# Kernel tuning notes

Measured on AMD Instinct MI355X. Metric: run time of the kernel, lower is better.

The kernel has to match this reference:

```python
import jax, jax.numpy as jnp
import numpy as np

A = 128   # image height (x_shape[0])
B = 128   # image width  (x_shape[1]); must equal A for the matmuls to type-check
N = 64    # glimpse size
H_DIM = 512
BATCH = 2048


def _filterbanks(params):
    """Vectorized Gaussian filterbank construction (replaces the per-column loop).
    params: (5,) = [gt_X, gt_Y, log_var, log_dt, log_gamma].
    gt_X, gt_Y, d are detached in the original via fix_param() -> stop_gradient here.
    """
    gt_X = jax.lax.stop_gradient(params[0])
    gt_Y = jax.lax.stop_gradient(params[1])
    var = jnp.exp(params[2] + 1e-8)
    d = jax.lax.stop_gradient(jnp.exp(params[3]) * (max(A, B) - 1) / (N - 1))
    g_X = (A + 1) * (gt_X + 1) / 2
    g_Y = (B + 1) * (gt_Y + 1) / 2
    # torch.linspace(g + (-N/2-0.5)*d, g + (N-1-N/2-0.5)*d, N) == g + (i - N/2 - 0.5)*d
    offs = (jnp.arange(N, dtype=jnp.float32) - N / 2 - 0.5) * d
    mu_X = g_X + offs  # (N,)
    mu_Y = g_Y + offs  # (N,)
    a = jnp.arange(A, dtype=jnp.float32)
    b = jnp.arange(B, dtype=jnp.float32)
    F_X = jnp.exp(-(a[None, :] - mu_X[:, None]) ** 2 / (2 * var))  # (N, A)
    F_Y = jnp.exp(-(b[None, :] - mu_Y[:, None]) ** 2 / (2 * var))  # (N, B)
    # NOTE: original normalizes by the GLOBAL sum, not per-row.
    F_X = F_X / jnp.sum(F_X)
    F_Y = F_Y / jnp.sum(F_Y)
    return F_X, F_Y


def setup_inputs() -> dict:
    key = jax.random.key(0)
    k1, k2, k3, k4 = jax.random.split(key, 4)
    x = jax.random.normal(k1, (BATCH, A * B), dtype=jnp.float32)
    x_hat = jax.random.normal(k2, (BATCH, A * B), dtype=jnp.float32)
    h = jax.random.normal(k3, (BATCH, H_DIM), dtype=jnp.float32)
    # W_read: Linear(h_dim, 5). Small init so exp(log_var), exp(log_dt), exp(log_gamma) stay sane.
    W_read_w = jax.random.normal(k4, (5, H_DIM), dtype=jnp.float32) * 0.01
    W_read_b = jnp.zeros((5,), dtype=jnp.float32)
    return {"x": x, "x_hat": x_hat, "h": h, "W_read_w": W_read_w, "W_read_b": W_read_b}


def reference(x, x_hat, h, W_read_w, W_read_b):
    # params = W_read(h)[0]  -> uses only the first batch element's params (as in original)
    params = h[0] @ W_read_w.T + W_read_b  # (5,)
    gamma = jnp.exp(params[4])
    F_X, F_Y = _filterbanks(params)  # (N, A), (N, B)

    xr = x.reshape(-1, A, B)
    xh = x_hat.reshape(-1, A, B)
    # gamma * F_Y @ x @ F_X.T : (batch, N, N)
    x_filt = gamma * jnp.einsum('na,bac,mc->bnm', F_Y, xr, F_X)
    x_hat_filt = gamma * jnp.einsum('na,bac,mc->bnm', F_Y, xh, F_X)
    return jnp.concatenate([x_filt.reshape(-1, N * N), x_hat_filt.reshape(-1, N * N)], axis=1)
```

## Files before the change

kernel.cpp:

```cpp
#include <hip/hip_runtime.h>
#include <math.h>

#define A_DIM 128
#define N_G   64
#define HD    512
#define LDX   136

typedef short short8 __attribute__((ext_vector_type(8)));
typedef float floatx4 __attribute__((ext_vector_type(4)));

static __device__ __forceinline__ unsigned short f2bf(float f) {
  union { float f; unsigned u; } v; v.f = f;
  unsigned r = (v.u + 0x7fffu + ((v.u >> 16) & 1u)) >> 16;
  return (unsigned short)r;
}

__global__ __launch_bounds__(512) void fb_setup_kernel(
    const float* __restrict__ h, const float* __restrict__ Ww,
    const float* __restrict__ Wb, unsigned short* __restrict__ FXfrag,
    unsigned short* __restrict__ FYfrag) {
  __shared__ float p[5];
  __shared__ float redX[8], redY[8];
  __shared__ float invs[2];
  const int tid = threadIdx.x, wave = tid >> 6, lane = tid & 63;

  if (wave < 5) {
    float s = 0.f;
    for (int k = lane; k < HD; k += 64) s += h[k] * Ww[wave * HD + k];
#pragma unroll
    for (int off = 32; off > 0; off >>= 1) s += __shfl_down(s, off);
    if (lane == 0) p[wave] = s + Wb[wave];
  }
  __syncthreads();

  const float gX = 64.5f * (p[0] + 1.0f);
  const float gY = 64.5f * (p[1] + 1.0f);
  const float var = expf(p[2] + 1e-8f);
  const float dd = expf(p[3]) * (127.0f / 63.0f);
  const float gamma = expf(p[4]);
  const float two_var = 2.0f * var;

  float sX = 0.f, sY = 0.f;
  for (int i = tid; i < N_G * A_DIM; i += 512) {
    const int n = i >> 7, a = i & 127;
    const float off_n = ((float)n - 32.5f) * dd;
    const float tx = (float)a - (gX + off_n);
    const float ty = (float)a - (gY + off_n);
    sX += expf(-(tx * tx) / two_var);
    sY += expf(-(ty * ty) / two_var);
  }
#pragma unroll
  for (int off = 32; off > 0; off >>= 1) {
    sX += __shfl_down(sX, off);
    sY += __shfl_down(sY, off);
  }
  if (lane == 0) { redX[wave] = sX; redY[wave] = sY; }
  __syncthreads();
  if (tid == 0) {
    float tX = 0.f, tY = 0.f;
#pragma unroll
    for (int w = 0; w < 8; ++w) { tX += redX[w]; tY += redY[w]; }
    invs[0] = 1.0f / tX;
    invs[1] = gamma / tY;
  }
  __syncthreads();
  const float isX = invs[0], isYg = invs[1];

  for (int i = tid; i < 4 * 4 * 64 * 8; i += 512) {
    const int j = i & 7;
    const int ln = (i >> 3) & 63;
    const int kk = (i >> 9) & 3;
    const int tl = (i >> 11) & 3;
    const int mn = tl * 16 + (ln & 15);
    const int ca = kk * 32 + ((ln >> 4) << 3) + j;
    const float off_mn = ((float)mn - 32.5f) * dd;
    const float tx = (float)ca - (gX + off_mn);
    const float ty = (float)ca - (gY + off_mn);
    FXfrag[i] = f2bf(expf(-(tx * tx) / two_var) * isX);
    FYfrag[i] = f2bf(expf(-(ty * ty) / two_var) * isYg);
  }
}

__global__ __launch_bounds__(256) void glimpse_kernel(
    const float* __restrict__ x, const float* __restrict__ xh,
    const unsigned short* __restrict__ FXfrag,
    const unsigned short* __restrict__ FYfrag,
    float* __restrict__ out) {
  const int img = blockIdx.x;
  const int b = img >> 1, t = img & 1;
  const float* __restrict__ src = (t ? xh : x) + (size_t)b * (A_DIM * A_DIM);
  float* __restrict__ dst = out + (size_t)b * (2 * N_G * N_G) + t * (N_G * N_G);

  __shared__ __align__(16) unsigned short xs[A_DIM * LDX];
  __shared__ __align__(16) unsigned short us[N_G * LDX];

  const int tid = threadIdx.x;
  const int w = tid >> 6, lane = tid & 63;
  const int quad = lane >> 4, lm = lane & 15;

  {
    const float4* __restrict__ src4 = (const float4*)src;
#pragma unroll
    for (int it = 0; it < 16; ++it) {
      const int flat = it * 256 + tid;
      const int a = flat >> 5;
      const int c4 = (flat & 31) * 4;
      const float4 v = src4[flat];
      uint2 pk;
      pk.x = (unsigned)f2bf(v.x) | ((unsigned)f2bf(v.y) << 16);
      pk.y = (unsigned)f2bf(v.z) | ((unsigned)f2bf(v.w) << 16);
      *(uint2*)&xs[a * LDX + c4] = pk;
    }
  }
  __syncthreads();

  {
    floatx4 acc[2][4];
#pragma unroll
    for (int i = 0; i < 2; ++i)
#pragma unroll
      for (int j = 0; j < 4; ++j) acc[i][j] = (floatx4)0.f;

#pragma unroll
    for (int kk = 0; kk < 4; ++kk) {
      short8 aF[2], bF[4];
#pragma unroll
      for (int i = 0; i < 2; ++i)
        aF[i] = *(const short8*)&xs[((2 * w + i) * 16 + lm) * LDX + kk * 32 + quad * 8];
#pragma unroll
      for (int j = 0; j < 4; ++j)
        bF[j] = *(const short8*)(FXfrag + ((size_t)(j * 4 + kk) * 64 + lane) * 8);
#pragma unroll
      for (int i = 0; i < 2; ++i)
#pragma unroll
        for (int j = 0; j < 4; ++j)
          acc[i][j] = __builtin_amdgcn_mfma_f32_16x16x32_bf16(aF[i], bF[j], acc[i][j], 0, 0, 0);
    }

#pragma unroll
    for (int i = 0; i < 2; ++i)
#pragma unroll
      for (int j = 0; j < 4; ++j) {
        uint2 pk;
        pk.x = (unsigned)f2bf(acc[i][j][0]) | ((unsigned)f2bf(acc[i][j][1]) << 16);
        pk.y = (unsigned)f2bf(acc[i][j][2]) | ((unsigned)f2bf(acc[i][j][3]) << 16);
        *(uint2*)&us[(j * 16 + lm) * LDX + (2 * w + i) * 16 + quad * 4] = pk;
      }
  }
  __syncthreads();

  {
    floatx4 acc2[4];
#pragma unroll
    for (int j = 0; j < 4; ++j) acc2[j] = (floatx4)0.f;

#pragma unroll
    for (int kk = 0; kk < 4; ++kk) {
      const short8 aF = *(const short8*)(FYfrag + ((size_t)(w * 4 + kk) * 64 + lane) * 8);
#pragma unroll
      for (int mt = 0; mt < 4; ++mt) {
        const short8 bF = *(const short8*)&us[(mt * 16 + lm) * LDX + kk * 32 + quad * 8];
        acc2[mt] = __builtin_amdgcn_mfma_f32_16x16x32_bf16(aF, bF, acc2[mt], 0, 0, 0);
      }
    }

#pragma unroll
    for (int mt = 0; mt < 4; ++mt)
#pragma unroll
      for (int r = 0; r < 4; ++r)
        dst[(w * 16 + quad * 4 + r) * N_G + mt * 16 + lm] = acc2[mt][r];
  }
}

extern "C" void kernel_launch(void* const* d_in, const int* in_sizes, int n_in,
                              void* d_out, int out_size, void* d_ws, size_t ws_size,
                              hipStream_t stream) {
  const float* x  = (const float*)d_in[0];
  const float* xh = (const float*)d_in[1];
  const float* h  = (const float*)d_in[2];
  const float* Ww = (const float*)d_in[3];
  const float* Wb = (const float*)d_in[4];
  float* out = (float*)d_out;

  unsigned short* FXfrag = (unsigned short*)d_ws;
  unsigned short* FYfrag = FXfrag + 4 * 4 * 64 * 8;

  fb_setup_kernel<<<1, 512, 0, stream>>>(h, Ww, Wb, FXfrag, FYfrag);
  glimpse_kernel<<<4096, 256, 0, stream>>>(x, xh, FXfrag, FYfrag, out);
}
```

Measured before the change: 313.4 us.

## Load MFMA A-fragments straight from global, drop xs staging, XOR-swizzle us

```diff
diff --git a/kernel.cpp b/kernel.cpp
--- a/kernel.cpp
+++ b/kernel.cpp
@@ -4,7 +4,6 @@
 #define A_DIM 128
 #define N_G   64
 #define HD    512
-#define LDX   136
 
 typedef short short8 __attribute__((ext_vector_type(8)));
 typedef float floatx4 __attribute__((ext_vector_type(4)));
@@ -13,6 +12,15 @@
   union { float f; unsigned u; } v; v.f = f;
   unsigned r = (v.u + 0x7fffu + ((v.u >> 16) & 1u)) >> 16;
   return (unsigned short)r;
+}
+
+static __device__ __forceinline__ short8 pack8(float4 a, float4 b) {
+  short8 r;
+  r[0] = (short)f2bf(a.x); r[1] = (short)f2bf(a.y);
+  r[2] = (short)f2bf(a.z); r[3] = (short)f2bf(a.w);
+  r[4] = (short)f2bf(b.x); r[5] = (short)f2bf(b.y);
+  r[6] = (short)f2bf(b.z); r[7] = (short)f2bf(b.w);
+  return r;
 }
 
 __global__ __launch_bounds__(512) void fb_setup_kernel(
@@ -81,7 +89,7 @@
   }
 }
 
-__global__ __launch_bounds__(256) void glimpse_kernel(
+__global__ __launch_bounds__(256, 4) void glimpse_kernel(
     const float* __restrict__ x, const float* __restrict__ xh,
     const unsigned short* __restrict__ FXfrag,
     const unsigned short* __restrict__ FYfrag,
@@ -91,8 +99,7 @@
   const float* __restrict__ src = (t ? xh : x) + (size_t)b * (A_DIM * A_DIM);
   float* __restrict__ dst = out + (size_t)b * (2 * N_G * N_G) + t * (N_G * N_G);
 
-  __shared__ __align__(16) unsigned short xs[A_DIM * LDX];
-  __shared__ __align__(16) unsigned short us[N_G * LDX];
+  __shared__ __align__(16) unsigned short us[N_G * A_DIM];
 
   const int tid = threadIdx.x;
   const int w = tid >> 6, lane = tid & 63;
@@ -100,21 +107,20 @@
 
   {
     const float4* __restrict__ src4 = (const float4*)src;
+    short8 aF[2][4];
 #pragma unroll
-    for (int it = 0; it < 16; ++it) {
-      const int flat = it * 256 + tid;
-      const int a = flat >> 5;
-      const int c4 = (flat & 31) * 4;
-      const float4 v = src4[flat];
-      uint2 pk;
-      pk.x = (unsigned)f2bf(v.x) | ((unsigned)f2bf(v.y) << 16);
-      pk.y = (unsigned)f2bf(v.z) | ((unsigned)f2bf(v.w) << 16);
-      *(uint2*)&xs[a * LDX + c4] = pk;
+    for (int i = 0; i < 2; ++i) {
+      float4 u0[4], u1[4];
+#pragma unroll
+      for (int kk = 0; kk < 4; ++kk) {
+        const int idx = ((2 * w + i) * 16 + lm) * 32 + kk * 8 + quad * 2;
+        u0[kk] = src4[idx];
+        u1[kk] = src4[idx + 1];
+      }
+#pragma unroll
+      for (int kk = 0; kk < 4; ++kk) aF[i][kk] = pack8(u0[kk], u1[kk]);
     }
-  }
-  __syncthreads();
 
-  {
     floatx4 acc[2][4];
 #pragma unroll
     for (int i = 0; i < 2; ++i)
@@ -123,10 +129,7 @@
 
 #pragma unroll
     for (int kk = 0; kk < 4; ++kk) {
-      short8 aF[2], bF[4];
-#pragma unroll
-      for (int i = 0; i < 2; ++i)
-        aF[i] = *(const short8*)&xs[((2 * w + i) * 16 + lm) * LDX + kk * 32 + quad * 8];
+      short8 bF[4];
 #pragma unroll
       for (int j = 0; j < 4; ++j)
         bF[j] = *(const short8*)(FXfrag + ((size_t)(j * 4 + kk) * 64 + lane) * 8);
@@ -134,18 +137,21 @@
       for (int i = 0; i < 2; ++i)
 #pragma unroll
         for (int j = 0; j < 4; ++j)
-          acc[i][j] = __builtin_amdgcn_mfma_f32_16x16x32_bf16(aF[i], bF[j], acc[i][j], 0, 0, 0);
+          acc[i][j] = __builtin_amdgcn_mfma_f32_16x16x32_bf16(aF[i][kk], bF[j], acc[i][j], 0, 0, 0);
     }
 
 #pragma unroll
-    for (int i = 0; i < 2; ++i)
+    for (int i = 0; i < 2; ++i) {
+      const int ch = (2 * w + i) * 2 + (quad >> 1);
+      const int half = (quad & 1) * 4;
 #pragma unroll
       for (int j = 0; j < 4; ++j) {
         uint2 pk;
         pk.x = (unsigned)f2bf(acc[i][j][0]) | ((unsigned)f2bf(acc[i][j][1]) << 16);
         pk.y = (unsigned)f2bf(acc[i][j][2]) | ((unsigned)f2bf(acc[i][j][3]) << 16);
-        *(uint2*)&us[(j * 16 + lm) * LDX + (2 * w + i) * 16 + quad * 4] = pk;
+        *(uint2*)&us[(j * 16 + lm) * A_DIM + ((ch ^ lm) << 3) + half] = pk;
       }
+    }
   }
   __syncthreads();
 
@@ -159,7 +165,8 @@
       const short8 aF = *(const short8*)(FYfrag + ((size_t)(w * 4 + kk) * 64 + lane) * 8);
 #pragma unroll
       for (int mt = 0; mt < 4; ++mt) {
-        const short8 bF = *(const short8*)&us[(mt * 16 + lm) * LDX + kk * 32 + quad * 8];
+        const int ch = (kk * 4 + quad) ^ lm;
+        const short8 bF = *(const short8*)&us[(mt * 16 + lm) * A_DIM + (ch << 3)];
         acc2[mt] = __builtin_amdgcn_mfma_f32_16x16x32_bf16(aF, bF, acc2[mt], 0, 0, 0);
       }
     }
```

Result: no change. 311.6 us (-0.6%).
